# Performance work log

Hardware: AMD Instinct MI355X
Metric: run time of the kernel (lower is better)

The kernel has to match this reference:

```python
import jax, jax.numpy as jnp
import numpy as np

B, S, T = 32, 64, 64
E, H = 512, 1024   # H == 2*E required by the dot-product attention
VS, VT = 32000, 32000


def setup_inputs() -> dict:
    key = jax.random.key(0)
    ks = jax.random.split(key, 12)
    sc = 0.02
    return {
        "target_sentences": jax.random.randint(ks[0], (B, T), 0, VT),
        "target_lengths": jax.random.randint(ks[1], (B,), 1, T + 1),
        "source_lengths": jax.random.randint(ks[2], (B,), 1, S + 1),
        "source_sentences": jax.random.randint(ks[3], (B, S), 0, VS),
        "positions": jax.random.randint(ks[4], (B, S), 0, S + 1),
        "max_len": S,
        "target_len": T,
        "force": 1,
        "enc_emb": jax.random.normal(ks[5], (VS, E), jnp.float32) * sc,
        "pos_emb": jax.random.normal(ks[6], (S + 1, E), jnp.float32) * sc,
        "dec_emb": jax.random.normal(ks[7], (VT, E), jnp.float32) * sc,
        "W_h0": jax.random.normal(ks[8], (H, 2 * E), jnp.float32) * sc,
        "b_h0": jnp.zeros((H,), jnp.float32),
        "W_ih": jax.random.normal(ks[9], (4 * H, 3 * E), jnp.float32) * sc,
        "W_hh": jax.random.normal(ks[10], (4 * H, H), jnp.float32) * sc,
        "b_ih": jnp.zeros((4 * H,), jnp.float32),
        "b_hh": jnp.zeros((4 * H,), jnp.float32),
        "W_out": jax.random.normal(ks[11], (VT, 2 * E), jnp.float32) * sc,
        "b_out": jnp.zeros((VT,), jnp.float32),
    }


def reference(target_sentences, target_lengths, source_lengths, source_sentences,
              positions, max_len, target_len, force,
              enc_emb, pos_emb, dec_emb, W_h0, b_h0,
              W_ih, W_hh, b_ih, b_hh, W_out, b_out):
    # encoder: word + positional embeddings concatenated -> [B,S,2E]
    enc = jnp.concatenate([enc_emb[source_sentences], pos_emb[positions]], axis=2)
    words = dec_emb[target_sentences]                 # [B,T,E]
    h0 = jnp.mean(enc, axis=1) @ W_h0.T + b_h0        # [B,H]
    # length mask over source positions
    mask = (jnp.arange(max_len)[None, :] < source_lengths[:, None]).astype(enc.dtype)  # [B,S]

    def step(carry, w):
        h, c = carry                                  # [B,H] each
        # masked dot-product attention of decoder state against encoder outputs
        energy = jnp.einsum('bsd,bd->bs', enc, h)     # H == 2E
        attn = jax.nn.softmax(energy, axis=-1)
        masked = attn * mask
        attn_n = masked / jnp.sum(masked, axis=-1, keepdims=True)
        ctx = jnp.einsum('bs,bsd->bd', attn_n, enc)   # [B,2E]
        # LSTM cell (torch gate order i,f,g,o), teacher forcing
        x = jnp.concatenate([w, ctx], axis=-1)        # [B,3E]
        gates = x @ W_ih.T + b_ih + h @ W_hh.T + b_hh # [B,4H]
        i, f, g, o = jnp.split(gates, 4, axis=-1)
        c = jax.nn.sigmoid(f) * c + jax.nn.sigmoid(i) * jnp.tanh(g)
        h = jax.nn.sigmoid(o) * jnp.tanh(c)
        return (h, c), h

    _, hs = jax.lax.scan(step, (h0, h0), jnp.swapaxes(words, 0, 1))  # hs: [T,B,H]
    out = jnp.einsum('tbh,vh->btv', hs, W_out) + b_out               # [B,T,VT]
    return out
```

## Files before the change

### kernel.cpp

```cpp
#include <hip/hip_runtime.h>
#include <cstdint>
#include <cstddef>

#define B_  32
#define S_  64
#define T_  64
#define E_  512
#define H_  1024
#define VT_ 32000

using short8  = __attribute__((ext_vector_type(8))) short;
using floatx4 = __attribute__((ext_vector_type(4))) float;
using us4     = __attribute__((ext_vector_type(4))) unsigned short;

__device__ __forceinline__ unsigned short f2bf(float f) {
  unsigned int u = __builtin_bit_cast(unsigned int, f);
  u = u + 0x7fffu + ((u >> 16) & 1u);
  return (unsigned short)(u >> 16);
}
__device__ __forceinline__ float sigf(float x) { return 1.f / (1.f + __expf(-x)); }

__global__ void build_enc(const int* __restrict__ ss, const int* __restrict__ pp,
                          const float* __restrict__ enc_emb, const float* __restrict__ pos_emb,
                          float* __restrict__ enc) {
  int row = blockIdx.x, tid = threadIdx.x;
  int tok = ss[row], pos = pp[row];
  float2 a = *(const float2*)&enc_emb[(size_t)tok * E_ + tid * 2];
  float2 p = *(const float2*)&pos_emb[(size_t)pos * E_ + tid * 2];
  *(float2*)&enc[(size_t)row * 1024 + tid * 2]       = a;
  *(float2*)&enc[(size_t)row * 1024 + 512 + tid * 2] = p;
}

__global__ void enc_mean(const float* __restrict__ enc, float* __restrict__ em) {
  int b = blockIdx.x, tid = threadIdx.x;
  float4 acc = {0, 0, 0, 0};
  for (int s = 0; s < S_; ++s) {
    float4 v = *(const float4*)&enc[((size_t)b * S_ + s) * 1024 + tid * 4];
    acc.x += v.x; acc.y += v.y; acc.z += v.z; acc.w += v.w;
  }
  const float inv = 1.f / 64.f;
  acc.x *= inv; acc.y *= inv; acc.z *= inv; acc.w *= inv;
  *(float4*)&em[(size_t)b * 1024 + tid * 4] = acc;
}

__global__ __launch_bounds__(256) void h0_kernel(
    const float* __restrict__ em, const float* __restrict__ W_h0, const float* __restrict__ b_h0,
    float* __restrict__ hbuf, float* __restrict__ cbuf, unsigned short* __restrict__ xbuf) {
  int o = blockIdx.x * 4 + (threadIdx.x >> 6);
  int l = threadIdx.x & 63;
  int b = o >> 10, j = o & 1023;
  const float* wr = &W_h0[(size_t)j * 1024];
  const float* ev = &em[(size_t)b * 1024];
  float v = 0.f;
  #pragma unroll
  for (int i = 0; i < 16; ++i) v += wr[l + i * 64] * ev[l + i * 64];
  #pragma unroll
  for (int off = 32; off; off >>= 1) v += __shfl_down(v, off);
  if (l == 0) {
    v += b_h0[j];
    hbuf[b * 1024 + j] = v;
    cbuf[b * 1024 + j] = v;
    xbuf[b * 2048 + 1024 + j] = f2bf(v);
  }
}

__global__ void build_words(const int* __restrict__ ts, const float* __restrict__ dec_emb,
                            unsigned short* __restrict__ words_bf) {
  int bi = blockIdx.x;
  int b = bi >> 6, t = bi & 63;
  int tok = ts[bi];
  int m = t * 32 + b;
  int tid = threadIdx.x;
  float2 v = *(const float2*)&dec_emb[(size_t)tok * E_ + tid * 2];
  words_bf[(size_t)m * E_ + tid * 2]     = f2bf(v.x);
  words_bf[(size_t)m * E_ + tid * 2 + 1] = f2bf(v.y);
}

__global__ void cast_wstep(const float* __restrict__ W_ih, const float* __restrict__ W_hh,
                           unsigned short* __restrict__ Wstep) {
  int r = blockIdx.x, c = threadIdx.x * 4;
  float4 a = *(const float4*)&W_ih[(size_t)r * 1536 + 512 + c];
  float4 h = *(const float4*)&W_hh[(size_t)r * 1024 + c];
  us4 va; va[0] = f2bf(a.x); va[1] = f2bf(a.y); va[2] = f2bf(a.z); va[3] = f2bf(a.w);
  us4 vh; vh[0] = f2bf(h.x); vh[1] = f2bf(h.y); vh[2] = f2bf(h.z); vh[3] = f2bf(h.w);
  *(us4*)&Wstep[(size_t)r * 2048 + c]        = va;
  *(us4*)&Wstep[(size_t)r * 2048 + 1024 + c] = vh;
}

__global__ __launch_bounds__(256) void gemm_bf16(
    const unsigned short* __restrict__ A, int lda,
    const float* __restrict__ Bw, int ldb,
    float* __restrict__ C, int ldc,
    const float* __restrict__ bias1, const float* __restrict__ bias2,
    int K, int mode) {
  __shared__ unsigned short sA[128 * 32];
  __shared__ unsigned short sB[128 * 32];
  const int tid = threadIdx.x;
  const int n0 = blockIdx.x * 128, m0 = blockIdx.y * 128;
  const int w = tid >> 6, l = tid & 63;
  const int wm = w >> 1, wn = w & 1;
  const int l15 = l & 15, q = l >> 4;

  floatx4 acc[4][4];
  #pragma unroll
  for (int i = 0; i < 4; ++i)
    #pragma unroll
    for (int j = 0; j < 4; ++j) acc[i][j] = (floatx4){0.f, 0.f, 0.f, 0.f};

  for (int k0 = 0; k0 < K; k0 += 32) {
    __syncthreads();
    #pragma unroll
    for (int p = 0; p < 2; ++p) {
      int idx8 = p * 256 + tid;
      int row = idx8 >> 2, kc = (idx8 & 3) << 3;
      *(short8*)&sA[row * 32 + kc] =
          *(const short8*)&A[(size_t)(m0 + row) * lda + k0 + kc];
    }
    #pragma unroll
    for (int p = 0; p < 4; ++p) {
      int idx4 = p * 256 + tid;
      int row = idx4 >> 3, kc = (idx4 & 7) << 2;
      float4 f = *(const float4*)&Bw[(size_t)(n0 + row) * ldb + k0 + kc];
      us4 v; v[0] = f2bf(f.x); v[1] = f2bf(f.y); v[2] = f2bf(f.z); v[3] = f2bf(f.w);
      *(us4*)&sB[row * 32 + kc] = v;
    }
    __syncthreads();
    short8 af[4], bf8[4];
    #pragma unroll
    for (int mt = 0; mt < 4; ++mt)
      af[mt] = *(short8*)&sA[(wm * 64 + mt * 16 + l15) * 32 + q * 8];
    #pragma unroll
    for (int nt = 0; nt < 4; ++nt)
      bf8[nt] = *(short8*)&sB[(wn * 64 + nt * 16 + l15) * 32 + q * 8];
    #pragma unroll
    for (int mt = 0; mt < 4; ++mt)
      #pragma unroll
      for (int nt = 0; nt < 4; ++nt)
        acc[mt][nt] = __builtin_amdgcn_mfma_f32_16x16x32_bf16(af[mt], bf8[nt], acc[mt][nt], 0, 0, 0);
  }

  #pragma unroll
  for (int mt = 0; mt < 4; ++mt)
    #pragma unroll
    for (int nt = 0; nt < 4; ++nt)
      #pragma unroll
      for (int r = 0; r < 4; ++r) {
        int m = m0 + wm * 64 + mt * 16 + q * 4 + r;
        int n = n0 + wn * 64 + nt * 16 + l15;
        float v = acc[mt][nt][r];
        if (bias1) v += bias1[n];
        if (bias2) v += bias2[n];
        if (mode == 0) {
          C[(size_t)m * ldc + n] = v;
        } else {
          int b = m & 31, t = m >> 5;
          C[(size_t)(b * 64 + t) * ldc + n] = v;
        }
      }
}

__global__ __launch_bounds__(256) void attn_ctx(
    const float* __restrict__ enc, const float* __restrict__ hbuf,
    const int* __restrict__ slen, unsigned short* __restrict__ xbuf) {
  __shared__ float hsh[1024];
  __shared__ float esh[64];
  __shared__ float ash[64];
  int b = blockIdx.x, tid = threadIdx.x;
  *(float4*)&hsh[tid * 4] = *(const float4*)&hbuf[(size_t)b * 1024 + tid * 4];
  __syncthreads();
  int w = tid >> 6, l = tid & 63;
  for (int si = 0; si < 16; ++si) {
    int s = w * 16 + si;
    const float* er = &enc[((size_t)b * S_ + s) * 1024];
    float v = 0.f;
    #pragma unroll
    for (int i = 0; i < 16; ++i) v += er[l + i * 64] * hsh[l + i * 64];
    #pragma unroll
    for (int off = 32; off; off >>= 1) v += __shfl_down(v, off);
    if (l == 0) esh[s] = v;
  }
  __syncthreads();
  if (tid < 64) {
    int len = slen[b];
    float e = (tid < len) ? esh[tid] : -1e30f;
    float m = e;
    #pragma unroll
    for (int off = 32; off; off >>= 1) m = fmaxf(m, __shfl_down(m, off));
    m = __shfl(m, 0);
    float p = (tid < len) ? __expf(e - m) : 0.f;
    float s = p;
    #pragma unroll
    for (int off = 32; off; off >>= 1) s += __shfl_down(s, off);
    s = __shfl(s, 0);
    ash[tid] = p / s;
  }
  __syncthreads();
  float4 acc = {0, 0, 0, 0};
  const float* eb = &enc[(size_t)b * S_ * 1024 + tid * 4];
  for (int s = 0; s < S_; ++s) {
    float a = ash[s];
    float4 ev = *(const float4*)&eb[(size_t)s * 1024];
    acc.x += a * ev.x; acc.y += a * ev.y; acc.z += a * ev.z; acc.w += a * ev.w;
  }
  int d0 = tid * 4;
  us4 v; v[0] = f2bf(acc.x); v[1] = f2bf(acc.y); v[2] = f2bf(acc.z); v[3] = f2bf(acc.w);
  *(us4*)&xbuf[(size_t)b * 2048 + d0] = v;
}

__global__ __launch_bounds__(256) void step_gates(
    const unsigned short* __restrict__ xbuf,
    const unsigned short* __restrict__ Wstep,
    const float* __restrict__ gw,
    float* __restrict__ hbuf, float* __restrict__ cbuf,
    unsigned short* __restrict__ hs,
    int t) {
  __shared__ float red[4 * 512];
  const int tid = threadIdx.x;
  const int w = tid >> 6, l = tid & 63;
  const int l15 = l & 15, q = l >> 4;
  const int u0 = blockIdx.x * 4;
  const int rn = (l15 >> 2) * 1024 + u0 + (l15 & 3);
  floatx4 acc0 = (floatx4){0.f, 0.f, 0.f, 0.f};
  floatx4 acc1 = (floatx4){0.f, 0.f, 0.f, 0.f};
  const int kbase = w * 512;
  #pragma unroll 4
  for (int ks = 0; ks < 16; ++ks) {
    int k0 = kbase + ks * 32 + q * 8;
    short8 b8 = *(const short8*)&Wstep[(size_t)rn * 2048 + k0];
    short8 a0 = *(const short8*)&xbuf[(size_t)l15 * 2048 + k0];
    short8 a1 = *(const short8*)&xbuf[(size_t)(16 + l15) * 2048 + k0];
    acc0 = __builtin_amdgcn_mfma_f32_16x16x32_bf16(a0, b8, acc0, 0, 0, 0);
    acc1 = __builtin_amdgcn_mfma_f32_16x16x32_bf16(a1, b8, acc1, 0, 0, 0);
  }
  #pragma unroll
  for (int r = 0; r < 4; ++r) {
    red[w * 512 + (q * 4 + r) * 16 + l15]        = acc0[r];
    red[w * 512 + (16 + q * 4 + r) * 16 + l15]   = acc1[r];
  }
  __syncthreads();
  if (tid < 128) {
    int b = tid >> 2, ui = tid & 3;
    float g4[4];
    #pragma unroll
    for (int g = 0; g < 4; ++g) {
      int n = g * 4 + ui;
      float s = red[b * 16 + n] + red[512 + b * 16 + n] +
                red[1024 + b * 16 + n] + red[1536 + b * 16 + n];
      s += gw[(size_t)(t * 32 + b) * 4096 + g * 1024 + u0 + ui];
      g4[g] = s;
    }
    int u = u0 + ui;
    float c_old = cbuf[b * 1024 + u];
    float fi = sigf(g4[0]);
    float ff = sigf(g4[1]);
    float gg = tanhf(g4[2]);
    float fo = sigf(g4[3]);
    float cn = ff * c_old + fi * gg;
    float hn = fo * tanhf(cn);
    cbuf[b * 1024 + u] = cn;
    hbuf[b * 1024 + u] = hn;
    unsigned short hb = f2bf(hn);
    const_cast<unsigned short*>(xbuf)[b * 2048 + 1024 + u] = hb;
    hs[(size_t)(t * 32 + b) * 1024 + u] = hb;
  }
}

extern "C" void kernel_launch(void* const* d_in, const int* in_sizes, int n_in,
                              void* d_out, int out_size, void* d_ws, size_t ws_size,
                              hipStream_t stream) {
  const int*   ts     = (const int*)d_in[0];
  const int*   slen   = (const int*)d_in[2];
  const int*   ss     = (const int*)d_in[3];
  const int*   pp     = (const int*)d_in[4];
  const float* enc_emb = (const float*)d_in[8];
  const float* pos_emb = (const float*)d_in[9];
  const float* dec_emb = (const float*)d_in[10];
  const float* W_h0   = (const float*)d_in[11];
  const float* b_h0   = (const float*)d_in[12];
  const float* W_ih   = (const float*)d_in[13];
  const float* W_hh   = (const float*)d_in[14];
  const float* b_ih   = (const float*)d_in[15];
  const float* b_hh   = (const float*)d_in[16];
  const float* W_out  = (const float*)d_in[17];
  const float* b_out  = (const float*)d_in[18];
  float* out = (float*)d_out;

  char* base = (char*)d_ws;
  size_t off = 0;
  auto carve = [&](size_t bytes) { void* p = base + off; off += (bytes + 255) & ~(size_t)255; return p; };
  float*          enc      = (float*)carve((size_t)B_ * S_ * 1024 * 4);
  float*          em       = (float*)carve((size_t)B_ * 1024 * 4);
  float*          hbuf     = (float*)carve((size_t)B_ * 1024 * 4);
  float*          cbuf     = (float*)carve((size_t)B_ * 1024 * 4);
  unsigned short* xbuf     = (unsigned short*)carve((size_t)B_ * 2048 * 2);
  unsigned short* words_bf = (unsigned short*)carve((size_t)2048 * E_ * 2);
  unsigned short* Wstep    = (unsigned short*)carve((size_t)4096 * 2048 * 2);
  float*          gw       = (float*)carve((size_t)2048 * 4096 * 4);
  unsigned short* hs       = (unsigned short*)carve((size_t)2048 * 1024 * 2);

  build_enc  <<<B_ * S_, 256, 0, stream>>>(ss, pp, enc_emb, pos_emb, enc);
  enc_mean   <<<B_,      256, 0, stream>>>(enc, em);
  h0_kernel  <<<(B_ * H_) / 4, 256, 0, stream>>>(em, W_h0, b_h0, hbuf, cbuf, xbuf);
  build_words<<<B_ * T_, 256, 0, stream>>>(ts, dec_emb, words_bf);
  cast_wstep <<<4096,    256, 0, stream>>>(W_ih, W_hh, Wstep);
  gemm_bf16<<<dim3(4096 / 128, 2048 / 128), 256, 0, stream>>>(
      words_bf, E_, W_ih, 1536, gw, 4096, b_ih, b_hh, E_, 0);

  for (int t = 0; t < T_; ++t) {
    attn_ctx  <<<B_,  256, 0, stream>>>(enc, hbuf, slen, xbuf);
    step_gates<<<256, 256, 0, stream>>>(xbuf, Wstep, gw, hbuf, cbuf, hs, t);
  }

  gemm_bf16<<<dim3(VT_ / 128, 2048 / 128), 256, 0, stream>>>(
      hs, H_, W_out, H_, out, VT_, b_out, nullptr, H_, 1);
}
```

Baseline: 2.223 ms.

## Fuse recurrence into persistent grid-barrier kernel and rework GEMM with async LDS loads

```diff
diff --git a/kernel.cpp b/kernel.cpp
--- a/kernel.cpp
+++ b/kernel.cpp
@@ -19,6 +19,24 @@
   return (unsigned short)(u >> 16);
 }
 __device__ __forceinline__ float sigf(float x) { return 1.f / (1.f + __expf(-x)); }
+
+__device__ __forceinline__ void glds16(const void* g, void* l) {
+  __builtin_amdgcn_global_load_lds(
+      (const __attribute__((address_space(1))) unsigned int*)g,
+      (__attribute__((address_space(3))) unsigned int*)l, 16, 0, 0);
+}
+
+__device__ __forceinline__ void gridbar(unsigned int* bar, unsigned int target) {
+  __syncthreads();
+  if (threadIdx.x == 0) {
+    __threadfence();
+    __hip_atomic_fetch_add(bar, 1u, __ATOMIC_RELAXED, __HIP_MEMORY_SCOPE_AGENT);
+    while (__hip_atomic_load(bar, __ATOMIC_RELAXED, __HIP_MEMORY_SCOPE_AGENT) < target)
+      __builtin_amdgcn_s_sleep(2);
+    __threadfence();
+  }
+  __syncthreads();
+}
 
 __global__ void build_enc(const int* __restrict__ ss, const int* __restrict__ pp,
                           const float* __restrict__ enc_emb, const float* __restrict__ pos_emb,
@@ -87,19 +105,34 @@
   *(us4*)&Wstep[(size_t)r * 2048 + 1024 + c] = vh;
 }
 
-__global__ __launch_bounds__(256) void gemm_bf16(
+__global__ void cast_wout(const float* __restrict__ W, unsigned short* __restrict__ Wb) {
+  size_t i = ((size_t)blockIdx.x * 256 + threadIdx.x) * 4;
+  float4 f = *(const float4*)&W[i];
+  us4 v; v[0] = f2bf(f.x); v[1] = f2bf(f.y); v[2] = f2bf(f.z); v[3] = f2bf(f.w);
+  *(us4*)&Wb[i] = v;
+}
+
+__global__ __launch_bounds__(256) void gemm_bb(
     const unsigned short* __restrict__ A, int lda,
-    const float* __restrict__ Bw, int ldb,
+    const void* __restrict__ Bv, int ldb, int bfmt,
     float* __restrict__ C, int ldc,
     const float* __restrict__ bias1, const float* __restrict__ bias2,
     int K, int mode) {
-  __shared__ unsigned short sA[128 * 32];
-  __shared__ unsigned short sB[128 * 32];
+  __shared__ unsigned short sA[128 * 64];
+  __shared__ unsigned short sB[128 * 64];
   const int tid = threadIdx.x;
-  const int n0 = blockIdx.x * 128, m0 = blockIdx.y * 128;
+  const int nwg  = gridDim.x * gridDim.y;
+  const int flat = blockIdx.y * gridDim.x + blockIdx.x;
+  const int u    = (flat & 7) * (nwg >> 3) + (flat >> 3);
+  const int by   = u % gridDim.y;
+  const int bx   = u / gridDim.y;
+  const int n0 = bx * 128, m0 = by * 128;
   const int w = tid >> 6, l = tid & 63;
   const int wm = w >> 1, wn = w & 1;
   const int l15 = l & 15, q = l >> 4;
+  const int xs = (l15 & 7) << 3;
+  const int gr = l >> 3;
+  const int gk = (l & 7) << 3;
 
   floatx4 acc[4][4];
   #pragma unroll
@@ -107,36 +140,52 @@
     #pragma unroll
     for (int j = 0; j < 4; ++j) acc[i][j] = (floatx4){0.f, 0.f, 0.f, 0.f};
 
-  for (int k0 = 0; k0 < K; k0 += 32) {
+  for (int k0 = 0; k0 < K; k0 += 64) {
     __syncthreads();
     #pragma unroll
-    for (int p = 0; p < 2; ++p) {
-      int idx8 = p * 256 + tid;
-      int row = idx8 >> 2, kc = (idx8 & 3) << 3;
-      *(short8*)&sA[row * 32 + kc] =
-          *(const short8*)&A[(size_t)(m0 + row) * lda + k0 + kc];
-    }
+    for (int p = 0; p < 4; ++p) {
+      int inst = w * 4 + p;
+      int row = inst * 8 + gr;
+      int kk = gk ^ ((row & 7) << 3);
+      glds16(&A[(size_t)(m0 + row) * lda + k0 + kk], &sA[inst * 512]);
+    }
+    if (bfmt) {
+      const unsigned short* Bw = (const unsigned short*)Bv;
+      #pragma unroll
+      for (int p = 0; p < 4; ++p) {
+        int inst = w * 4 + p;
+        int row = inst * 8 + gr;
+        int kk = gk ^ ((row & 7) << 3);
+        glds16(&Bw[(size_t)(n0 + row) * ldb + k0 + kk], &sB[inst * 512]);
+      }
+    } else {
+      const float* Bw = (const float*)Bv;
+      #pragma unroll
+      for (int p = 0; p < 8; ++p) {
+        int idx4 = p * 256 + tid;
+        int row = idx4 >> 4, kc = (idx4 & 15) << 2;
+        float4 f = *(const float4*)&Bw[(size_t)(n0 + row) * ldb + k0 + kc];
+        us4 v; v[0] = f2bf(f.x); v[1] = f2bf(f.y); v[2] = f2bf(f.z); v[3] = f2bf(f.w);
+        *(us4*)&sB[row * 64 + (kc ^ ((row & 7) << 3))] = v;
+      }
+    }
+    __syncthreads();
     #pragma unroll
-    for (int p = 0; p < 4; ++p) {
-      int idx4 = p * 256 + tid;
-      int row = idx4 >> 3, kc = (idx4 & 7) << 2;
-      float4 f = *(const float4*)&Bw[(size_t)(n0 + row) * ldb + k0 + kc];
-      us4 v; v[0] = f2bf(f.x); v[1] = f2bf(f.y); v[2] = f2bf(f.z); v[3] = f2bf(f.w);
-      *(us4*)&sB[row * 32 + kc] = v;
-    }
-    __syncthreads();
-    short8 af[4], bf8[4];
-    #pragma unroll
-    for (int mt = 0; mt < 4; ++mt)
-      af[mt] = *(short8*)&sA[(wm * 64 + mt * 16 + l15) * 32 + q * 8];
-    #pragma unroll
-    for (int nt = 0; nt < 4; ++nt)
-      bf8[nt] = *(short8*)&sB[(wn * 64 + nt * 16 + l15) * 32 + q * 8];
-    #pragma unroll
-    for (int mt = 0; mt < 4; ++mt)
+    for (int kk2 = 0; kk2 < 2; ++kk2) {
+      const int kr = (kk2 * 32 + q * 8) ^ xs;
+      short8 af[4], bf8[4];
+      #pragma unroll
+      for (int mt = 0; mt < 4; ++mt)
+        af[mt] = *(short8*)&sA[(wm * 64 + mt * 16 + l15) * 64 + kr];
       #pragma unroll
       for (int nt = 0; nt < 4; ++nt)
-        acc[mt][nt] = __builtin_amdgcn_mfma_f32_16x16x32_bf16(af[mt], bf8[nt], acc[mt][nt], 0, 0, 0);
+        bf8[nt] = *(short8*)&sB[(wn * 64 + nt * 16 + l15) * 64 + kr];
+      #pragma unroll
+      for (int mt = 0; mt < 4; ++mt)
+        #pragma unroll
+        for (int nt = 0; nt < 4; ++nt)
+          acc[mt][nt] = __builtin_amdgcn_mfma_f32_16x16x32_bf16(af[mt], bf8[nt], acc[mt][nt], 0, 0, 0);
+    }
   }
 
   #pragma unroll
@@ -159,109 +208,128 @@
       }
 }
 
-__global__ __launch_bounds__(256) void attn_ctx(
-    const float* __restrict__ enc, const float* __restrict__ hbuf,
-    const int* __restrict__ slen, unsigned short* __restrict__ xbuf) {
-  __shared__ float hsh[1024];
-  __shared__ float esh[64];
-  __shared__ float ash[64];
-  int b = blockIdx.x, tid = threadIdx.x;
-  *(float4*)&hsh[tid * 4] = *(const float4*)&hbuf[(size_t)b * 1024 + tid * 4];
-  __syncthreads();
-  int w = tid >> 6, l = tid & 63;
-  for (int si = 0; si < 16; ++si) {
-    int s = w * 16 + si;
-    const float* er = &enc[((size_t)b * S_ + s) * 1024];
-    float v = 0.f;
-    #pragma unroll
-    for (int i = 0; i < 16; ++i) v += er[l + i * 64] * hsh[l + i * 64];
-    #pragma unroll
-    for (int off = 32; off; off >>= 1) v += __shfl_down(v, off);
-    if (l == 0) esh[s] = v;
-  }
-  __syncthreads();
-  if (tid < 64) {
-    int len = slen[b];
-    float e = (tid < len) ? esh[tid] : -1e30f;
-    float m = e;
-    #pragma unroll
-    for (int off = 32; off; off >>= 1) m = fmaxf(m, __shfl_down(m, off));
-    m = __shfl(m, 0);
-    float p = (tid < len) ? __expf(e - m) : 0.f;
-    float s = p;
-    #pragma unroll
-    for (int off = 32; off; off >>= 1) s += __shfl_down(s, off);
-    s = __shfl(s, 0);
-    ash[tid] = p / s;
-  }
-  __syncthreads();
-  float4 acc = {0, 0, 0, 0};
-  const float* eb = &enc[(size_t)b * S_ * 1024 + tid * 4];
-  for (int s = 0; s < S_; ++s) {
-    float a = ash[s];
-    float4 ev = *(const float4*)&eb[(size_t)s * 1024];
-    acc.x += a * ev.x; acc.y += a * ev.y; acc.z += a * ev.z; acc.w += a * ev.w;
-  }
-  int d0 = tid * 4;
-  us4 v; v[0] = f2bf(acc.x); v[1] = f2bf(acc.y); v[2] = f2bf(acc.z); v[3] = f2bf(acc.w);
-  *(us4*)&xbuf[(size_t)b * 2048 + d0] = v;
-}
-
-__global__ __launch_bounds__(256) void step_gates(
-    const unsigned short* __restrict__ xbuf,
-    const unsigned short* __restrict__ Wstep,
-    const float* __restrict__ gw,
-    float* __restrict__ hbuf, float* __restrict__ cbuf,
-    unsigned short* __restrict__ hs,
-    int t) {
-  __shared__ float red[4 * 512];
+__global__ __launch_bounds__(256, 1) void recurrence(
+    const float* __restrict__ enc, float* __restrict__ hbuf, float* __restrict__ cbuf,
+    unsigned short* __restrict__ xb0, unsigned short* __restrict__ xb1,
+    const unsigned short* __restrict__ Wstep, const float* __restrict__ gw,
+    unsigned short* __restrict__ hs, const int* __restrict__ slen,
+    unsigned int* __restrict__ bar) {
+  __shared__ unsigned short wlds[16 * 2048];
+  __shared__ float red[2048];
+
   const int tid = threadIdx.x;
   const int w = tid >> 6, l = tid & 63;
   const int l15 = l & 15, q = l >> 4;
   const int u0 = blockIdx.x * 4;
-  const int rn = (l15 >> 2) * 1024 + u0 + (l15 & 3);
-  floatx4 acc0 = (floatx4){0.f, 0.f, 0.f, 0.f};
-  floatx4 acc1 = (floatx4){0.f, 0.f, 0.f, 0.f};
-  const int kbase = w * 512;
-  #pragma unroll 4
-  for (int ks = 0; ks < 16; ++ks) {
-    int k0 = kbase + ks * 32 + q * 8;
-    short8 b8 = *(const short8*)&Wstep[(size_t)rn * 2048 + k0];
-    short8 a0 = *(const short8*)&xbuf[(size_t)l15 * 2048 + k0];
-    short8 a1 = *(const short8*)&xbuf[(size_t)(16 + l15) * 2048 + k0];
-    acc0 = __builtin_amdgcn_mfma_f32_16x16x32_bf16(a0, b8, acc0, 0, 0, 0);
-    acc1 = __builtin_amdgcn_mfma_f32_16x16x32_bf16(a1, b8, acc1, 0, 0, 0);
-  }
-  #pragma unroll
-  for (int r = 0; r < 4; ++r) {
-    red[w * 512 + (q * 4 + r) * 16 + l15]        = acc0[r];
-    red[w * 512 + (16 + q * 4 + r) * 16 + l15]   = acc1[r];
-  }
-  __syncthreads();
-  if (tid < 128) {
-    int b = tid >> 2, ui = tid & 3;
-    float g4[4];
-    #pragma unroll
-    for (int g = 0; g < 4; ++g) {
-      int n = g * 4 + ui;
-      float s = red[b * 16 + n] + red[512 + b * 16 + n] +
-                red[1024 + b * 16 + n] + red[1536 + b * 16 + n];
-      s += gw[(size_t)(t * 32 + b) * 4096 + g * 1024 + u0 + ui];
-      g4[g] = s;
-    }
-    int u = u0 + ui;
-    float c_old = cbuf[b * 1024 + u];
-    float fi = sigf(g4[0]);
-    float ff = sigf(g4[1]);
-    float gg = tanhf(g4[2]);
-    float fo = sigf(g4[3]);
-    float cn = ff * c_old + fi * gg;
-    float hn = fo * tanhf(cn);
-    cbuf[b * 1024 + u] = cn;
-    hbuf[b * 1024 + u] = hn;
-    unsigned short hb = f2bf(hn);
-    const_cast<unsigned short*>(xbuf)[b * 2048 + 1024 + u] = hb;
-    hs[(size_t)(t * 32 + b) * 1024 + u] = hb;
+
+  #pragma unroll
+  for (int ii = 0; ii < 16; ++ii) {
+    int idx = ii * 256 + tid;
+    int n = idx >> 8;
+    int kc = (idx & 255) << 3;
+    int rn = (n >> 2) * 1024 + u0 + (n & 3);
+    short8 v = *(const short8*)&Wstep[(size_t)rn * 2048 + kc];
+    *(short8*)&wlds[n * 2048 + (kc ^ ((n & 7) << 3))] = v;
+  }
+
+  const int lenb = (blockIdx.x < 32) ? slen[blockIdx.x] : 0;
+  float* hsh  = red;
+  float* esh  = red + 1024;
+  float* ashp = red + 1088;
+
+  unsigned int bt = 0;
+
+  for (int t = 0; t < 64; ++t) {
+    unsigned short* xc = (t & 1) ? xb1 : xb0;
+    unsigned short* xn = (t & 1) ? xb0 : xb1;
+
+    if (blockIdx.x < 32) {
+      int b = blockIdx.x;
+      *(float4*)&hsh[tid * 4] = *(const float4*)&hbuf[(size_t)b * 1024 + tid * 4];
+      __syncthreads();
+      for (int si = 0; si < 16; ++si) {
+        int s = w * 16 + si;
+        const float* er = &enc[((size_t)b * S_ + s) * 1024];
+        float v = 0.f;
+        #pragma unroll
+        for (int i = 0; i < 16; ++i) v += er[l + i * 64] * hsh[l + i * 64];
+        #pragma unroll
+        for (int off = 32; off; off >>= 1) v += __shfl_down(v, off);
+        if (l == 0) esh[s] = v;
+      }
+      __syncthreads();
+      if (tid < 64) {
+        float e = (tid < lenb) ? esh[tid] : -1e30f;
+        float m = e;
+        #pragma unroll
+        for (int off = 32; off; off >>= 1) m = fmaxf(m, __shfl_down(m, off));
+        m = __shfl(m, 0);
+        float p = (tid < lenb) ? __expf(e - m) : 0.f;
+        float s = p;
+        #pragma unroll
+        for (int off = 32; off; off >>= 1) s += __shfl_down(s, off);
+        s = __shfl(s, 0);
+        ashp[tid] = p / s;
+      }
+      __syncthreads();
+      float4 acc = {0, 0, 0, 0};
+      const float* eb = &enc[(size_t)b * S_ * 1024 + tid * 4];
+      for (int s = 0; s < S_; ++s) {
+        float a = ashp[s];
+        float4 ev = *(const float4*)&eb[(size_t)s * 1024];
+        acc.x += a * ev.x; acc.y += a * ev.y; acc.z += a * ev.z; acc.w += a * ev.w;
+      }
+      us4 v; v[0] = f2bf(acc.x); v[1] = f2bf(acc.y); v[2] = f2bf(acc.z); v[3] = f2bf(acc.w);
+      *(us4*)&xc[b * 2048 + tid * 4] = v;
+    }
+    bt += 256; gridbar(bar, bt);
+
+    {
+      floatx4 acc0 = (floatx4){0.f, 0.f, 0.f, 0.f};
+      floatx4 acc1 = (floatx4){0.f, 0.f, 0.f, 0.f};
+      const int kbase = w * 512;
+      #pragma unroll 4
+      for (int ks = 0; ks < 16; ++ks) {
+        int k0 = kbase + ks * 32 + q * 8;
+        short8 b8 = *(short8*)&wlds[l15 * 2048 + (k0 ^ ((l15 & 7) << 3))];
+        short8 a0 = *(const short8*)&xc[(size_t)l15 * 2048 + k0];
+        short8 a1 = *(const short8*)&xc[(size_t)(16 + l15) * 2048 + k0];
+        acc0 = __builtin_amdgcn_mfma_f32_16x16x32_bf16(a0, b8, acc0, 0, 0, 0);
+        acc1 = __builtin_amdgcn_mfma_f32_16x16x32_bf16(a1, b8, acc1, 0, 0, 0);
+      }
+      #pragma unroll
+      for (int r = 0; r < 4; ++r) {
+        red[w * 512 + (q * 4 + r) * 16 + l15]      = acc0[r];
+        red[w * 512 + (16 + q * 4 + r) * 16 + l15] = acc1[r];
+      }
+      __syncthreads();
+      if (tid < 128) {
+        int b = tid >> 2, ui = tid & 3;
+        float g4[4];
+        #pragma unroll
+        for (int g = 0; g < 4; ++g) {
+          int n = g * 4 + ui;
+          float s = red[b * 16 + n] + red[512 + b * 16 + n] +
+                    red[1024 + b * 16 + n] + red[1536 + b * 16 + n];
+          s += gw[(size_t)(t * 32 + b) * 4096 + g * 1024 + u0 + ui];
+          g4[g] = s;
+        }
+        int u = u0 + ui;
+        float c_old = cbuf[b * 1024 + u];
+        float fi = sigf(g4[0]);
+        float ff = sigf(g4[1]);
+        float gg = tanhf(g4[2]);
+        float fo = sigf(g4[3]);
+        float cn = ff * c_old + fi * gg;
+        float hn = fo * tanhf(cn);
+        cbuf[b * 1024 + u] = cn;
+        hbuf[b * 1024 + u] = hn;
+        unsigned short hb = f2bf(hn);
+        xn[b * 2048 + 1024 + u] = hb;
+        hs[(size_t)(t * 32 + b) * 1024 + u] = hb;
+      }
+    }
+    bt += 256; gridbar(bar, bt);
   }
 }
 
@@ -292,25 +360,31 @@
   float*          em       = (float*)carve((size_t)B_ * 1024 * 4);
   float*          hbuf     = (float*)carve((size_t)B_ * 1024 * 4);
   float*          cbuf     = (float*)carve((size_t)B_ * 1024 * 4);
-  unsigned short* xbuf     = (unsigned short*)carve((size_t)B_ * 2048 * 2);
+  unsigned short* xb0      = (unsigned short*)carve((size_t)B_ * 2048 * 2);
+  unsigned short* xb1      = (unsigned short*)carve((size_t)B_ * 2048 * 2);
   unsigned short* words_bf = (unsigned short*)carve((size_t)2048 * E_ * 2);
   unsigned short* Wstep    = (unsigned short*)carve((size_t)4096 * 2048 * 2);
   float*          gw       = (float*)carve((size_t)2048 * 4096 * 4);
   unsigned short* hs       = (unsigned short*)carve((size_t)2048 * 1024 * 2);
+  unsigned int*   bar      = (unsigned int*)carve(256);
+  unsigned short* Wob      = (unsigned short*)carve((size_t)VT_ * 1024 * 2);
+  const bool haveWob = (off <= ws_size);
+
+  hipMemsetAsync(bar, 0, sizeof(unsigned int), stream);
 
   build_enc  <<<B_ * S_, 256, 0, stream>>>(ss, pp, enc_emb, pos_emb, enc);
   enc_mean   <<<B_,      256, 0, stream>>>(enc, em);
-  h0_kernel  <<<(B_ * H_) / 4, 256, 0, stream>>>(em, W_h0, b_h0, hbuf, cbuf, xbuf);
+  h0_kernel  <<<(B_ * H_) / 4, 256, 0, stream>>>(em, W_h0, b_h0, hbuf, cbuf, xb0);
   build_words<<<B_ * T_, 256, 0, stream>>>(ts, dec_emb, words_bf);
   cast_wstep <<<4096,    256, 0, stream>>>(W_ih, W_hh, Wstep);
-  gemm_bf16<<<dim3(4096 / 128, 2048 / 128), 256, 0, stream>>>(
-      words_bf, E_, W_ih, 1536, gw, 4096, b_ih, b_hh, E_, 0);
-
-  for (int t = 0; t < T_; ++t) {
-    attn_ctx  <<<B_,  256, 0, stream>>>(enc, hbuf, slen, xbuf);
-    step_gates<<<256, 256, 0, stream>>>(xbuf, Wstep, gw, hbuf, cbuf, hs, t);
-  }
-
-  gemm_bf16<<<dim3(VT_ / 128, 2048 / 128), 256, 0, stream>>>(
-      hs, H_, W_out, H_, out, VT_, b_out, nullptr, H_, 1);
-}
+  if (haveWob) cast_wout<<<VT_, 256, 0, stream>>>(W_out, Wob);
+
+  gemm_bb<<<dim3(4096 / 128, 2048 / 128), 256, 0, stream>>>(
+      words_bf, E_, (const void*)W_ih, 1536, 0, gw, 4096, b_ih, b_hh, E_, 0);
+
+  recurrence<<<256, 256, 0, stream>>>(enc, hbuf, cbuf, xb0, xb1, Wstep, gw, hs, slen, bar);
+
+  gemm_bb<<<dim3(VT_ / 128, 2048 / 128), 256, 0, stream>>>(
+      hs, H_, haveWob ? (const void*)Wob : (const void*)W_out, H_, haveWob ? 1 : 0,
+      out, VT_, b_out, nullptr, H_, 1);
+}
```

Result: slower. 4.021 ms (+80.9%).
